# Performance work log

Hardware: AMD Instinct MI355X
Metric: run time of the kernel (lower is better)

Reference implementation:

```python
import jax, jax.numpy as jnp
import numpy as np

D = 512            # model size
H = 8              # num_heads
HD = D // H        # head_size = 64
WIN = 7            # num_keys (payload tokens per window)
QNB = 5            # query_nb for 'mean' aggregation
SCALE = D ** -0.5  # NOTE: torch module scales by size**-0.5, not head_size**-0.5
EPS = 1e-5


def setup_inputs() -> dict:
    key = jax.random.key(0)
    ks = jax.random.split(key, 12)
    B, M = 8, 4096
    w = lambda i: jax.random.normal(ks[i], (D, D), jnp.float32) * 0.02
    return {
        "k": jax.random.normal(ks[0], (B, M, D), jnp.float32),
        "v": jax.random.normal(ks[1], (B, M, D), jnp.float32),
        "q": jax.random.normal(ks[2], (B, M, D), jnp.float32),
        "query_len": 3584,
        "Wk": w(3), "bk": jnp.zeros((D,), jnp.float32),
        "Wv": w(4), "bv": jnp.zeros((D,), jnp.float32),
        "Wq": w(5), "bq": jnp.zeros((D,), jnp.float32),
        "ln_g": jnp.ones((D,), jnp.float32), "ln_b": jnp.zeros((D,), jnp.float32),
        "Wpq": w(6), "bpq": jnp.zeros((D,), jnp.float32),
        "Wpk": w(7), "bpk": jnp.zeros((D,), jnp.float32),
        "Wo": w(8), "bo": jnp.zeros((D,), jnp.float32),
    }


def reference(k, v, q, query_len, Wk, bk, Wv, bv, Wq, bq, ln_g, ln_b, Wpq, bpq, Wpk, bpk, Wo, bo):
    B, M, _ = k.shape
    win_num = -(-query_len // WIN)     # ceil
    per_win = M // win_num

    k = k @ Wk + bk
    v = v @ Wv + bv
    q = q @ Wq + bq

    # 'mean' query aggregation: AvgPool1d(kernel=QNB, stride=1, pad=QNB//2),
    # count_include_pad=True => always divide by QNB (zero-padded)
    qp = jnp.pad(q, ((0, 0), (QNB // 2, QNB // 2), (0, 0)))
    q = sum(qp[:, j:j + M] for j in range(QNB)) / QNB

    # ---- stage 1: DSA (local attention inside each window of per_win tokens)
    resh = lambda x: x.reshape(B, win_num, per_win, H, HD).transpose(0, 1, 3, 2, 4)
    dq, dk, dv = resh(q), resh(k), resh(v)                       # [B,W,H,p,hd]
    attn = jax.nn.softmax(jnp.einsum('bwhqd,bwhkd->bwhqk', dq, dk) * SCALE, axis=-1)
    out = jnp.einsum('bwhqk,bwhkd->bwhqd', attn, dv)
    out = out.transpose(0, 1, 3, 2, 4).reshape(B, win_num, per_win, D)

    win_tok = out[:, :, 0, :]          # [B, W, D] window summary tokens
    attn_x = out[:, :, 1:, :]

    # LayerNorm + exact GELU on window tokens
    mu = win_tok.mean(-1, keepdims=True)
    var = ((win_tok - mu) ** 2).mean(-1, keepdims=True)
    win_tok = (win_tok - mu) / jnp.sqrt(var + EPS) * ln_g + ln_b
    win_tok = jax.nn.gelu(win_tok, approximate=False)

    # ---- stage 2: PSA (attention over window summary tokens)
    pq = (win_tok @ Wpq + bpq).reshape(B, win_num, H, HD).transpose(0, 2, 1, 3)  # [B,H,W,hd]
    pk = (win_tok @ Wpk + bpk).reshape(B, win_num, H, HD).transpose(0, 2, 1, 3)
    pv = attn_x.reshape(B, win_num, WIN, H, HD).transpose(0, 3, 1, 2, 4)
    pv = pv.reshape(B, H, win_num, WIN * HD)

    pattn = jax.nn.softmax(jnp.einsum('bhqd,bhkd->bhqk', pq, pk) * SCALE, axis=-1)
    pout = jnp.einsum('bhqk,bhkd->bhqd', pattn, pv)
    pout = pout.transpose(0, 2, 1, 3).reshape(B, win_num, H, WIN, HD)
    pout = pout.transpose(0, 1, 3, 2, 4).reshape(B, win_num, WIN, D)

    out = (pout + attn_x).reshape(B, win_num * WIN, D)[:, :query_len, :]
    return out @ Wo + bo
```

## Files before the change

kernel.cpp:

```cpp
#include <hip/hip_runtime.h>
#include <hip/hip_bf16.h>
#include <math.h>

#define SCALE_ 0.04419417382415922f
#define EPS_  1e-5f

typedef unsigned short u16;
typedef __attribute__((ext_vector_type(8))) short     bf16x8;
typedef __attribute__((ext_vector_type(4))) float     f32x4;
typedef __attribute__((ext_vector_type(8))) unsigned short u16x8;
typedef __attribute__((ext_vector_type(4))) unsigned short u16x4;

__device__ __forceinline__ u16 f2b(float f) {
  union { float f; unsigned int u; } x; x.f = f;
  unsigned int u = x.u;
  return (u16)((u + 0x7FFFu + ((u >> 16) & 1u)) >> 16);
}
__device__ __forceinline__ float b2f(u16 h) {
  union { unsigned int u; float f; } x; x.u = ((unsigned int)h) << 16;
  return x.f;
}
__device__ __forceinline__ void gload_lds16(const void* g, void* l) {
  __builtin_amdgcn_global_load_lds(
      (const __attribute__((address_space(1))) void*)g,
      (__attribute__((address_space(3))) void*)l, 16, 0, 0);
}

__global__ __launch_bounds__(256) void wconv(
    const float* W0, const float* W1, const float* W2,
    const float* W3, const float* W4, const float* W5, u16* wt)
{
  const float* W;
  switch (blockIdx.z) {
    case 0: W = W0; break; case 1: W = W1; break; case 2: W = W2; break;
    case 3: W = W3; break; case 4: W = W4; break; default: W = W5; break;
  }
  u16* Wt = wt + (size_t)blockIdx.z * 262144;
  const int k0 = blockIdx.x * 64, n0 = blockIdx.y * 64;
  __shared__ float T[64][68];
  const int tid = threadIdx.x;
#pragma unroll
  for (int it = 0; it < 4; ++it) {
    int L = it * 256 + tid;
    int r = L >> 4, cg = L & 15;
    float4 v = *reinterpret_cast<const float4*>(W + (size_t)(k0 + r) * 512 + n0 + cg * 4);
    T[r][cg * 4 + 0] = v.x; T[r][cg * 4 + 1] = v.y;
    T[r][cg * 4 + 2] = v.z; T[r][cg * 4 + 3] = v.w;
  }
  __syncthreads();
#pragma unroll
  for (int it = 0; it < 2; ++it) {
    int L = it * 256 + tid;
    int rn = L >> 3, kg = L & 7;
    u16x8 o;
#pragma unroll
    for (int e = 0; e < 8; ++e) o[e] = f2b(T[kg * 8 + e][rn]);
    *(u16x8*)(Wt + (size_t)(n0 + rn) * 512 + k0 + kg * 8) = o;
  }
}

__global__ __launch_bounds__(512) void gemm_proj(
    const float* A0, const u16* Bt0, const float* bi0, u16* C0,
    const float* A1, const u16* Bt1, const float* bi1, u16* C1,
    const float* A2, const u16* Bt2, const float* bi2, u16* C2)
{
  const float *A, *bias; const u16* Bt; u16* C;
  if (blockIdx.z == 0)      { A = A0; Bt = Bt0; bias = bi0; C = C0; }
  else if (blockIdx.z == 1) { A = A1; Bt = Bt1; bias = bi1; C = C1; }
  else                      { A = A2; Bt = Bt2; bias = bi2; C = C2; }

  __shared__ u16 As[8192];
  __shared__ u16 Bs[32768];
  const int tid = threadIdx.x;
  const int lane = tid & 63, wid = tid >> 6;
  const int wr = wid >> 2, wcn = wid & 3;
  const int l15 = lane & 15, lh = lane >> 4, l7 = lane & 7;
  const int m0 = blockIdx.x * 128;

  const f32x4 fz = {0.f, 0.f, 0.f, 0.f};
  f32x4 acc[4][8];
#pragma unroll
  for (int m = 0; m < 4; ++m)
#pragma unroll
    for (int n = 0; n < 8; ++n) acc[m][n] = fz;

  int aoff[2], boff[2];
#pragma unroll
  for (int kh = 0; kh < 2; ++kh) {
    int slot = ((kh * 4 + lh) ^ l7) << 4;
    aoff[kh] = (wr * 64 + l15) * 128 + slot;
    boff[kh] = (wcn * 128 + l15) * 128 + slot;
  }

  for (int k0 = 0; k0 < 512; k0 += 64) {
    __syncthreads();
#pragma unroll
    for (int it = 0; it < 8; ++it) {
      int L = it * 512 + tid;
      int r = L >> 3, s = L & 7;
      int c = s ^ (r & 7);
      gload_lds16(Bt + (size_t)r * 512 + k0 + c * 8,
                  (char*)Bs + (it * 512 + wid * 64) * 16);
    }
    float4 xa[2], xb[2];
#pragma unroll
    for (int it = 0; it < 2; ++it) {
      int L = it * 512 + tid;
      int r = L >> 3, s = L & 7;
      int c = s ^ (r & 7);
      const float* ga = A + (size_t)(m0 + r) * 512 + k0 + c * 8;
      xa[it] = *reinterpret_cast<const float4*>(ga);
      xb[it] = *reinterpret_cast<const float4*>(ga + 4);
    }
#pragma unroll
    for (int it = 0; it < 2; ++it) {
      int L = it * 512 + tid;
      u16x8 o;
      o[0] = f2b(xa[it].x); o[1] = f2b(xa[it].y);
      o[2] = f2b(xa[it].z); o[3] = f2b(xa[it].w);
      o[4] = f2b(xb[it].x); o[5] = f2b(xb[it].y);
      o[6] = f2b(xb[it].z); o[7] = f2b(xb[it].w);
      *(u16x8*)((char*)As + L * 16) = o;
    }
    __syncthreads();
#pragma unroll
    for (int kh = 0; kh < 2; ++kh) {
      bf16x8 af[4], bfr[8];
#pragma unroll
      for (int m = 0; m < 4; ++m)
        af[m] = *(const bf16x8*)((const char*)As + aoff[kh] + m * 2048);
#pragma unroll
      for (int n = 0; n < 8; ++n)
        bfr[n] = *(const bf16x8*)((const char*)Bs + boff[kh] + n * 2048);
#pragma unroll
      for (int m = 0; m < 4; ++m)
#pragma unroll
        for (int n = 0; n < 8; ++n)
          acc[m][n] = __builtin_amdgcn_mfma_f32_16x16x32_bf16(af[m], bfr[n], acc[m][n], 0, 0, 0);
    }
  }

  const int gn0 = wcn * 128 + l15;
  float bv[8];
#pragma unroll
  for (int n = 0; n < 8; ++n) bv[n] = bias[gn0 + n * 16];
#pragma unroll
  for (int m = 0; m < 4; ++m)
#pragma unroll
    for (int reg = 0; reg < 4; ++reg) {
      int gm = m0 + wr * 64 + m * 16 + lh * 4 + reg;
#pragma unroll
      for (int n = 0; n < 8; ++n)
        C[(size_t)gm * 512 + gn0 + n * 16] = f2b(acc[m][n][reg] + bv[n]);
    }
}

__global__ __launch_bounds__(512) void gemm_out(
    const u16* __restrict__ A, const u16* __restrict__ Bt,
    const float* __restrict__ bias, float* __restrict__ C)
{
  __shared__ u16 As[2][4096];
  __shared__ u16 Bs[2][16384];
  const int tid = threadIdx.x;
  const int lane = tid & 63, wid = tid >> 6;
  const int wr = wid >> 2, wcn = wid & 3;
  const int l15 = lane & 15, lh = lane >> 4;
  const int sx = (l15 >> 1) & 3;
  const int m0 = blockIdx.x * 128;
  const int rr = tid >> 2, sp = tid & 3;
  const int ssw = sp ^ ((rr >> 1) & 3);

  const f32x4 fz = {0.f, 0.f, 0.f, 0.f};
  f32x4 acc[4][8];
#pragma unroll
  for (int m = 0; m < 4; ++m)
#pragma unroll
    for (int n = 0; n < 8; ++n) acc[m][n] = fz;

  const int aoff0 = (wr * 64 + l15) * 64 + ((lh ^ sx) << 4);
  const int boff0 = (wcn * 128 + l15) * 64 + ((lh ^ sx) << 4);

  {
#pragma unroll
    for (int it = 0; it < 4; ++it)
      gload_lds16(Bt + (size_t)(it * 128 + rr) * 512 + ssw * 8,
                  (char*)Bs[0] + (it * 512 + wid * 64) * 16);
    gload_lds16(A + (size_t)(m0 + rr) * 512 + ssw * 8,
                (char*)As[0] + (wid * 64) * 16);
  }
  __syncthreads();

#pragma unroll 2
  for (int t = 0; t < 16; ++t) {
    const int cur = t & 1, nxt = cur ^ 1;
    if (t < 15) {
      const int k0 = (t + 1) * 32;
#pragma unroll
      for (int it = 0; it < 4; ++it)
        gload_lds16(Bt + (size_t)(it * 128 + rr) * 512 + k0 + ssw * 8,
                    (char*)Bs[nxt] + (it * 512 + wid * 64) * 16);
      gload_lds16(A + (size_t)(m0 + rr) * 512 + k0 + ssw * 8,
                  (char*)As[nxt] + (wid * 64) * 16);
    }
    bf16x8 af[4], bfr[8];
#pragma unroll
    for (int m = 0; m < 4; ++m)
      af[m] = *(const bf16x8*)((const char*)As[cur] + aoff0 + m * 1024);
#pragma unroll
    for (int n = 0; n < 8; ++n)
      bfr[n] = *(const bf16x8*)((const char*)Bs[cur] + boff0 + n * 1024);
#pragma unroll
    for (int m = 0; m < 4; ++m)
#pragma unroll
      for (int n = 0; n < 8; ++n)
        acc[m][n] = __builtin_amdgcn_mfma_f32_16x16x32_bf16(af[m], bfr[n], acc[m][n], 0, 0, 0);
    __syncthreads();
  }

  const int gn0 = wcn * 128 + l15;
  float bv[8];
#pragma unroll
  for (int n = 0; n < 8; ++n) bv[n] = bias[gn0 + n * 16];
#pragma unroll
  for (int m = 0; m < 4; ++m)
#pragma unroll
    for (int reg = 0; reg < 4; ++reg) {
      int gm = m0 + wr * 64 + m * 16 + lh * 4 + reg;
#pragma unroll
      for (int n = 0; n < 8; ++n)
        C[(size_t)gm * 512 + gn0 + n * 16] = acc[m][n][reg] + bv[n];
    }
}

__global__ __launch_bounds__(256) void gemm_pp(
    const u16* __restrict__ A,
    const u16* __restrict__ Bt0, const float* __restrict__ bi0, u16* __restrict__ C0,
    const u16* __restrict__ Bt1, const float* __restrict__ bi1, u16* __restrict__ C1)
{
  const u16* Bt; const float* bias; u16* C;
  if (blockIdx.z == 0) { Bt = Bt0; bias = bi0; C = C0; }
  else                 { Bt = Bt1; bias = bi1; C = C1; }

  __shared__ u16 As[8192];
  __shared__ u16 Bs[8192];
  const int tid = threadIdx.x;
  const int lane = tid & 63, wid = tid >> 6;
  const int wr = wid >> 1, wc = wid & 1;
  const int l15 = lane & 15, lh = lane >> 4, l7 = lane & 7;
  const int m0 = blockIdx.x * 128, n0 = blockIdx.y * 128;

  const f32x4 fz = {0.f, 0.f, 0.f, 0.f};
  f32x4 acc[4][4];
#pragma unroll
  for (int m = 0; m < 4; ++m)
#pragma unroll
    for (int n = 0; n < 4; ++n) acc[m][n] = fz;

  int aoff[2], boff[2];
#pragma unroll
  for (int kh = 0; kh < 2; ++kh) {
    int slot = ((kh * 4 + lh) ^ l7) << 4;
    aoff[kh] = (wr * 64 + l15) * 128 + slot;
    boff[kh] = (wc * 64 + l15) * 128 + slot;
  }

  for (int k0 = 0; k0 < 512; k0 += 64) {
    __syncthreads();
#pragma unroll
    for (int it = 0; it < 4; ++it) {
      int L = it * 256 + tid;
      int r = L >> 3, s = L & 7;
      int c = s ^ (r & 7);
      gload_lds16(A  + (size_t)(m0 + r) * 512 + k0 + c * 8,
                  (char*)As + (it * 256 + wid * 64) * 16);
      gload_lds16(Bt + (size_t)(n0 + r) * 512 + k0 + c * 8,
                  (char*)Bs + (it * 256 + wid * 64) * 16);
    }
    __syncthreads();
#pragma unroll
    for (int kh = 0; kh < 2; ++kh) {
      bf16x8 af[4], bfr[4];
#pragma unroll
      for (int m = 0; m < 4; ++m)
        af[m] = *(const bf16x8*)((const char*)As + aoff[kh] + m * 2048);
#pragma unroll
      for (int n = 0; n < 4; ++n)
        bfr[n] = *(const bf16x8*)((const char*)Bs + boff[kh] + n * 2048);
#pragma unroll
      for (int m = 0; m < 4; ++m)
#pragma unroll
        for (int n = 0; n < 4; ++n)
          acc[m][n] = __builtin_amdgcn_mfma_f32_16x16x32_bf16(af[m], bfr[n], acc[m][n], 0, 0, 0);
    }
  }

  const int gn0 = n0 + wc * 64 + l15;
  float bv[4];
#pragma unroll
  for (int n = 0; n < 4; ++n) bv[n] = bias[gn0 + n * 16];
#pragma unroll
  for (int m = 0; m < 4; ++m)
#pragma unroll
    for (int reg = 0; reg < 4; ++reg) {
      int gm = m0 + wr * 64 + m * 16 + lh * 4 + reg;
#pragma unroll
      for (int n = 0; n < 4; ++n)
        C[(size_t)gm * 512 + gn0 + n * 16] = f2b(acc[m][n][reg] + bv[n]);
    }
}

__global__ __launch_bounds__(256) void qk_mfma(
    const u16* __restrict__ pq, const u16* __restrict__ pk,
    u16* __restrict__ expS, float* __restrict__ rsumP)
{
  __shared__ u16 As[8192];
  __shared__ u16 Bs[8192];
  const int tid = threadIdx.x;
  const int lane = tid & 63, wid = tid >> 6;
  const int wr = wid >> 1, wc = wid & 1;
  const int l15 = lane & 15, lh = lane >> 4, l7 = lane & 7;
  const int bh = blockIdx.x & 63;
  const int sidx = blockIdx.x >> 6;
  const int b = bh >> 3, h = bh & 7;
  const int wq0 = (sidx & 3) * 128, wk0 = (sidx >> 2) * 128;

  const f32x4 fz = {0.f, 0.f, 0.f, 0.f};
  f32x4 acc[4][4];
#pragma unroll
  for (int m = 0; m < 4; ++m)
#pragma unroll
    for (int n = 0; n < 4; ++n) acc[m][n] = fz;

#pragma unroll
  for (int it = 0; it < 4; ++it) {
    int L = it * 256 + tid;
    int r = L >> 3, s = L & 7;
    int c = s ^ (r & 7);
    gload_lds16(pq + ((size_t)b * 512 + wq0 + r) * 512 + h * 64 + c * 8,
                (char*)As + (it * 256 + wid * 64) * 16);
    gload_lds16(pk + ((size_t)b * 512 + wk0 + r) * 512 + h * 64 + c * 8,
                (char*)Bs + (it * 256 + wid * 64) * 16);
  }
  __syncthreads();

#pragma unroll
  for (int kh = 0; kh < 2; ++kh) {
    int slot = ((kh * 4 + lh) ^ l7) << 4;
    int aoff = (wr * 64 + l15) * 128 + slot;
    int boff = (wc * 64 + l15) * 128 + slot;
    bf16x8 af[4], bfr[4];
#pragma unroll
    for (int m = 0; m < 4; ++m)
      af[m] = *(const bf16x8*)((const char*)As + aoff + m * 2048);
#pragma unroll
    for (int n = 0; n < 4; ++n)
      bfr[n] = *(const bf16x8*)((const char*)Bs + boff + n * 2048);
#pragma unroll
    for (int m = 0; m < 4; ++m)
#pragma unroll
      for (int n = 0; n < 4; ++n)
        acc[m][n] = __builtin_amdgcn_mfma_f32_16x16x32_bf16(af[m], bfr[n], acc[m][n], 0, 0, 0);
  }

  const int gn0 = wk0 + wc * 64 + l15;
  float rs[4][4];
#pragma unroll
  for (int m = 0; m < 4; ++m)
#pragma unroll
    for (int reg = 0; reg < 4; ++reg) {
      int gm = wq0 + wr * 64 + m * 16 + lh * 4 + reg;
      float rsum = 0.0f;
#pragma unroll
      for (int n = 0; n < 4; ++n) {
        float e = expf(acc[m][n][reg] * SCALE_);
        rsum += e;
        expS[((size_t)bh * 512 + gm) * 512 + gn0 + n * 16] = f2b(e);
      }
      rs[m][reg] = rsum;
    }

#pragma unroll
  for (int m = 0; m < 4; ++m)
#pragma unroll
    for (int reg = 0; reg < 4; ++reg) {
      float v = rs[m][reg];
      v += __shfl_xor(v, 1);
      v += __shfl_xor(v, 2);
      v += __shfl_xor(v, 4);
      v += __shfl_xor(v, 8);
      rs[m][reg] = v;
    }
  if (l15 == 0) {
    const int p = (wk0 >> 6) + wc;
#pragma unroll
    for (int m = 0; m < 4; ++m)
#pragma unroll
      for (int reg = 0; reg < 4; ++reg) {
        int gm = wq0 + wr * 64 + m * 16 + lh * 4 + reg;
        rsumP[((size_t)bh * 8 + p) * 512 + gm] = rs[m][reg];
      }
  }
}

__global__ __launch_bounds__(64) void attn_win(
    const u16* kp, const u16* vp, const u16* qp0, u16* attn)
{
  const int h = blockIdx.x, w = blockIdx.y, b = blockIdx.z;
  const int t = threadIdx.x;
  __shared__ float ks[8][68], vs[8][68], qr[12][68], qs[8][68], Ps[8][9];
  const size_t base = ((size_t)b * 4096 + (size_t)w * 8) * 512 + h * 64;

  {
    int i = t >> 3, dg = t & 7;
    u16x8 kv = *(const u16x8*)(kp + base + (size_t)i * 512 + dg * 8);
    u16x8 vv = *(const u16x8*)(vp + base + (size_t)i * 512 + dg * 8);
#pragma unroll
    for (int e = 0; e < 8; ++e) {
      ks[i][dg * 8 + e] = b2f(kv[e]);
      vs[i][dg * 8 + e] = b2f(vv[e]);
    }
  }
#pragma unroll
  for (int l = 0; l < 2; ++l) {
    int L = t + l * 64;
    if (L < 96) {
      int i = L >> 3, dg = L & 7;
      int m = w * 8 - 2 + i;
      if (m >= 0 && m < 4096) {
        u16x8 qv = *(const u16x8*)(qp0 + ((size_t)b * 4096 + m) * 512 + h * 64 + dg * 8);
#pragma unroll
        for (int e = 0; e < 8; ++e) qr[i][dg * 8 + e] = b2f(qv[e]);
      } else {
#pragma unroll
        for (int e = 0; e < 8; ++e) qr[i][dg * 8 + e] = 0.0f;
      }
    }
  }
  __syncthreads();
#pragma unroll
  for (int j = 0; j < 8; ++j)
    qs[j][t] = 0.2f * (qr[j][t] + qr[j + 1][t] + qr[j + 2][t] + qr[j + 3][t] + qr[j + 4][t]);
  __syncthreads();

  const int qi = t >> 3, kj = t & 7;
  float s = 0.0f;
#pragma unroll
  for (int d = 0; d < 64; ++d) s = fmaf(qs[qi][d], ks[kj][d], s);
  s *= SCALE_;
  float mx = s;
  mx = fmaxf(mx, __shfl_xor(mx, 1));
  mx = fmaxf(mx, __shfl_xor(mx, 2));
  mx = fmaxf(mx, __shfl_xor(mx, 4));
  float e = expf(s - mx);
  float sum = e;
  sum += __shfl_xor(sum, 1);
  sum += __shfl_xor(sum, 2);
  sum += __shfl_xor(sum, 4);
  Ps[qi][kj] = e / sum;
  __syncthreads();

  float o[8];
#pragma unroll
  for (int c = 0; c < 8; ++c) o[c] = 0.0f;
#pragma unroll
  for (int tt = 0; tt < 8; ++tt) {
    float pw = Ps[qi][tt];
#pragma unroll
    for (int c = 0; c < 8; ++c) o[c] = fmaf(pw, vs[tt][kj * 8 + c], o[c]);
  }
  u16x8 ov;
#pragma unroll
  for (int c = 0; c < 8; ++c) ov[c] = f2b(o[c]);
  *(u16x8*)(attn + base + (size_t)qi * 512 + kj * 8) = ov;
}

__global__ __launch_bounds__(256) void pvt_build(const u16* attn, u16* pvT)
{
  const int bh = blockIdx.x;
  const int b = bh >> 3, h = bh & 7;
  const int w0 = blockIdx.y * 32;
  __shared__ u16 TL[448 * 40];
  const int tid = threadIdx.x;
#pragma unroll
  for (int it = 0; it < 8; ++it) {
    int L = it * 256 + tid;
    int dg = L & 7, r = L >> 3;
    int w2l = r >> 3, tt = r & 7;
    if (tt < 7) {
      int m = 8 * (w0 + w2l) + tt + 1;
      u16x8 v = *(const u16x8*)(attn + ((size_t)b * 4096 + m) * 512 + h * 64 + dg * 8);
#pragma unroll
      for (int e = 0; e < 8; ++e)
        TL[(tt * 64 + dg * 8 + e) * 40 + w2l] = v[e];
    }
  }
  __syncthreads();
#pragma unroll
  for (int it = 0; it < 7; ++it) {
    int L = it * 256 + tid;
    int n = L >> 2, seg = L & 3;
    u16x8 v = *(const u16x8*)(&TL[n * 40 + seg * 8]);
    *(u16x8*)(pvT + ((size_t)bh * 448 + n) * 512 + w0 + seg * 8) = v;
  }
}

__global__ __launch_bounds__(64) void ln_gelu(
    const u16* attn, const float* g, const float* be, u16* wt)
{
  const int r = blockIdx.x;
  const int b = r >> 9, w = r & 511;
  const int t = threadIdx.x;
  const u16* x = attn + (((size_t)b * 4096) + (size_t)w * 8) * 512;

  u16x8 v = *(const u16x8*)(x + t * 8);
  float xv[8];
  float s1 = 0.f, s2 = 0.f;
#pragma unroll
  for (int e = 0; e < 8; ++e) {
    xv[e] = b2f(v[e]);
    s1 += xv[e]; s2 += xv[e] * xv[e];
  }
#pragma unroll
  for (int off = 1; off < 64; off <<= 1) {
    s1 += __shfl_xor(s1, off);
    s2 += __shfl_xor(s2, off);
  }
  const float mu  = s1 * (1.0f / 512.0f);
  const float var = s2 * (1.0f / 512.0f) - mu * mu;
  const float inv = 1.0f / sqrtf(var + EPS_);

  const int d0 = t * 8;
  float4 g0 = *reinterpret_cast<const float4*>(g + d0);
  float4 g1 = *reinterpret_cast<const float4*>(g + d0 + 4);
  float4 b0 = *reinterpret_cast<const float4*>(be + d0);
  float4 b1 = *reinterpret_cast<const float4*>(be + d0 + 4);
  float gv[8] = {g0.x, g0.y, g0.z, g0.w, g1.x, g1.y, g1.z, g1.w};
  float bvv[8] = {b0.x, b0.y, b0.z, b0.w, b1.x, b1.y, b1.z, b1.w};
  const float k2 = 0.70710678118654752f;
  u16x8 ov;
#pragma unroll
  for (int e = 0; e < 8; ++e) {
    float y = (xv[e] - mu) * inv * gv[e] + bvv[e];
    ov[e] = f2b(0.5f * y * (1.0f + erff(y * k2)));
  }
  *(u16x8*)(wt + (size_t)r * 512 + d0) = ov;
}

__global__ __launch_bounds__(256) void rs_inv(const float* rsumP, float* rsinv)
{
  const int row = blockIdx.x * 256 + threadIdx.x;
  const int bh = row >> 9, wq = row & 511;
  float s = 0.f;
#pragma unroll
  for (int p = 0; p < 8; ++p)
    s += rsumP[((size_t)bh * 8 + p) * 512 + wq];
  rsinv[row] = 1.0f / s;
}

__global__ __launch_bounds__(256) void pv_mfma(
    const u16* __restrict__ expS, const u16* __restrict__ pvT,
    const float* __restrict__ rsinv, const u16* __restrict__ attn,
    u16* __restrict__ X2)
{
  __shared__ u16 As[8192];
  __shared__ u16 Bs[4096];
  const int tid = threadIdx.x;
  const int lane = tid & 63, wid = tid >> 6;
  const int wr = wid >> 1, wc = wid & 1;
  const int l15 = lane & 15, lh = lane >> 4, l7 = lane & 7;
  const int nt  = blockIdx.x >> 8;
  const int idx = blockIdx.x & 255;
  const int m0 = (idx & 3) * 128;
  const int bh = idx >> 2, b = bh >> 3, h = bh & 7;

  const f32x4 fz = {0.f, 0.f, 0.f, 0.f};
  f32x4 acc[4][2];
#pragma unroll
  for (int m = 0; m < 4; ++m)
#pragma unroll
    for (int n = 0; n < 2; ++n) acc[m][n] = fz;

  int aoff[2], boff[2];
#pragma unroll
  for (int kh = 0; kh < 2; ++kh) {
    int slot = ((kh * 4 + lh) ^ l7) << 4;
    aoff[kh] = (wr * 64 + l15) * 128 + slot;
    boff[kh] = (wc * 32 + l15) * 128 + slot;
  }

  for (int k0 = 0; k0 < 512; k0 += 64) {
    __syncthreads();
#pragma unroll
    for (int it = 0; it < 4; ++it) {
      int L = it * 256 + tid;
      int r = L >> 3, s = L & 7;
      int c = s ^ (r & 7);
      gload_lds16(expS + ((size_t)bh * 512 + m0 + r) * 512 + k0 + c * 8,
                  (char*)As + (it * 256 + wid * 64) * 16);
    }
#pragma unroll
    for (int it = 0; it < 2; ++it) {
      int L = it * 256 + tid;
      int r = L >> 3, s = L & 7;
      int c = s ^ (r & 7);
      gload_lds16(pvT + ((size_t)bh * 448 + nt * 64 + r) * 512 + k0 + c * 8,
                  (char*)Bs + (it * 256 + wid * 64) * 16);
    }
    __syncthreads();
#pragma unroll
    for (int kh = 0; kh < 2; ++kh) {
      bf16x8 af[4], bfr[2];
#pragma unroll
      for (int m = 0; m < 4; ++m)
        af[m] = *(const bf16x8*)((const char*)As + aoff[kh] + m * 2048);
#pragma unroll
      for (int n = 0; n < 2; ++n)
        bfr[n] = *(const bf16x8*)((const char*)Bs + boff[kh] + n * 2048);
#pragma unroll
      for (int m = 0; m < 4; ++m)
#pragma unroll
        for (int n = 0; n < 2; ++n)
          acc[m][n] = __builtin_amdgcn_mfma_f32_16x16x32_bf16(af[m], bfr[n], acc[m][n], 0, 0, 0);
    }
  }

#pragma unroll
  for (int m = 0; m < 4; ++m)
#pragma unroll
    for (int reg = 0; reg < 4; ++reg) {
      int gm = m0 + wr * 64 + m * 16 + lh * 4 + reg;
      float ri = rsinv[bh * 512 + gm];
#pragma unroll
      for (int n = 0; n < 2; ++n) {
        int d = wc * 32 + n * 16 + l15;
        float res = b2f(attn[((size_t)b * 4096 + gm * 8 + nt + 1) * 512 + h * 64 + d]);
        X2[((size_t)b * 3584 + gm * 7 + nt) * 512 + h * 64 + d] =
            f2b(acc[m][n][reg] * ri + res);
      }
    }
}

extern "C" void kernel_launch(void* const* d_in, const int* in_sizes, int n_in,
                              void* d_out, int out_size, void* d_ws, size_t ws_size,
                              hipStream_t stream)
{
  const float* k_in = (const float*)d_in[0];
  const float* v_in = (const float*)d_in[1];
  const float* q_in = (const float*)d_in[2];
  const float* Wk  = (const float*)d_in[4];
  const float* bk  = (const float*)d_in[5];
  const float* Wv  = (const float*)d_in[6];
  const float* bv  = (const float*)d_in[7];
  const float* Wq  = (const float*)d_in[8];
  const float* bq  = (const float*)d_in[9];
  const float* lng = (const float*)d_in[10];
  const float* lnb = (const float*)d_in[11];
  const float* Wpq = (const float*)d_in[12];
  const float* bpq = (const float*)d_in[13];
  const float* Wpk = (const float*)d_in[14];
  const float* bpk = (const float*)d_in[15];
  const float* Wo  = (const float*)d_in[16];
  const float* bo  = (const float*)d_in[17];
  float* out = (float*)d_out;

  char* ws = (char*)d_ws;
  const size_t MB = 1024 * 1024;
  u16* wtb  = (u16*)(ws);
  u16* kp   = (u16*)(ws + 16 * MB);
  u16* vp   = (u16*)(ws + 52 * MB);
  u16* qp0  = (u16*)(ws + 88 * MB);
  u16* attn = (u16*)(ws + 124 * MB);
  u16*   wt    = (u16*)(ws + 16 * MB);
  u16*   pq    = (u16*)(ws + 20 * MB);
  u16*   pk    = (u16*)(ws + 28 * MB);
  float* rsinv = (float*)(ws + 36 * MB);
  float* rsumP = (float*)(ws + 37 * MB);
  u16*   expS  = (u16*)(ws + 40 * MB);
  u16*   pvT   = (u16*)(ws + 76 * MB);
  u16*   X2    = (u16*)(ws + 160 * MB);

  u16* Wkt  = wtb;
  u16* Wvt  = wtb + 1 * 262144;
  u16* Wqt  = wtb + 2 * 262144;
  u16* Wpqt = wtb + 3 * 262144;
  u16* Wpkt = wtb + 4 * 262144;
  u16* Wot  = wtb + 5 * 262144;

  wconv<<<dim3(8, 8, 6), 256, 0, stream>>>(Wk, Wv, Wq, Wpq, Wpk, Wo, wtb);

  gemm_proj<<<dim3(256, 1, 3), 512, 0, stream>>>(
      k_in, Wkt, bk, kp,
      v_in, Wvt, bv, vp,
      q_in, Wqt, bq, qp0);

  attn_win<<<dim3(8, 512, 8), 64, 0, stream>>>(kp, vp, qp0, attn);
  pvt_build<<<dim3(64, 16), 256, 0, stream>>>(attn, pvT);
  ln_gelu<<<4096, 64, 0, stream>>>(attn, lng, lnb, wt);

  gemm_pp<<<dim3(32, 4, 2), 256, 0, stream>>>(
      wt, Wpqt, bpq, pq, Wpkt, bpk, pk);

  qk_mfma<<<1024, 256, 0, stream>>>(pq, pk, expS, rsumP);
  rs_inv<<<128, 256, 0, stream>>>(rsumP, rsinv);
  pv_mfma<<<1792, 256, 0, stream>>>(expS, pvT, rsinv, attn, X2);

  gemm_out<<<dim3(224, 1, 1), 512, 0, stream>>>(X2, Wot, bo, out);
}
```

Measured before the change: 278.0 us.

## Fuse PSA QK, softmax normalization and PV into one flash-style kernel

Replaces the three-kernel PSA stage (QK^T with exp written to global, row-sum reduction, P·V matmul) with a single fused kernel. Each block holds 128 query rows, loops over key tiles of 64, computes exp scores into LDS, then multiplies by the corresponding pvT tile, and normalizes by the row sum at the end. This avoids writing and re-reading the 32 MB bf16 expS buffer and removes two launches. In exchange, the grid shrinks to 256 blocks of 512 threads using about 96 KB of LDS each, with three barriers per key tile. No max subtraction is used, the same as before.

```diff
diff --git a/kernel.cpp b/kernel.cpp
--- a/kernel.cpp
+++ b/kernel.cpp
@@ -309,97 +309,134 @@
     }
 }
 
-__global__ __launch_bounds__(256) void qk_mfma(
+__global__ __launch_bounds__(512) void pattn(
     const u16* __restrict__ pq, const u16* __restrict__ pk,
-    u16* __restrict__ expS, float* __restrict__ rsumP)
-{
-  __shared__ u16 As[8192];
-  __shared__ u16 Bs[8192];
+    const u16* __restrict__ pvT, const u16* __restrict__ attn,
+    u16* __restrict__ X2)
+{
+  __shared__ u16 Aq[8192];
+  __shared__ u16 Bk[4096];
+  __shared__ u16 Pl[8192];
+  __shared__ u16 Vt[28672];
+  __shared__ float rsl[128];
+
   const int tid = threadIdx.x;
   const int lane = tid & 63, wid = tid >> 6;
-  const int wr = wid >> 1, wc = wid & 1;
+  const int wr = wid >> 2, wcn = wid & 3;
   const int l15 = lane & 15, lh = lane >> 4, l7 = lane & 7;
   const int bh = blockIdx.x & 63;
-  const int sidx = blockIdx.x >> 6;
+  const int wq0 = (blockIdx.x >> 6) * 128;
   const int b = bh >> 3, h = bh & 7;
-  const int wq0 = (sidx & 3) * 128, wk0 = (sidx >> 2) * 128;
 
   const f32x4 fz = {0.f, 0.f, 0.f, 0.f};
-  f32x4 acc[4][4];
-#pragma unroll
-  for (int m = 0; m < 4; ++m)
-#pragma unroll
-    for (int n = 0; n < 4; ++n) acc[m][n] = fz;
-
-#pragma unroll
-  for (int it = 0; it < 4; ++it) {
-    int L = it * 256 + tid;
+  f32x4 acc[4][7];
+#pragma unroll
+  for (int m = 0; m < 4; ++m)
+#pragma unroll
+    for (int n = 0; n < 7; ++n) acc[m][n] = fz;
+  float rs4[4] = {0.f, 0.f, 0.f, 0.f};
+
+#pragma unroll
+  for (int it = 0; it < 2; ++it) {
+    int L = it * 512 + tid;
     int r = L >> 3, s = L & 7;
     int c = s ^ (r & 7);
     gload_lds16(pq + ((size_t)b * 512 + wq0 + r) * 512 + h * 64 + c * 8,
-                (char*)As + (it * 256 + wid * 64) * 16);
-    gload_lds16(pk + ((size_t)b * 512 + wk0 + r) * 512 + h * 64 + c * 8,
-                (char*)Bs + (it * 256 + wid * 64) * 16);
+                (char*)Aq + L * 16);
+  }
+
+  int slotk[2];
+#pragma unroll
+  for (int kh = 0; kh < 2; ++kh) slotk[kh] = ((kh * 4 + lh) ^ l7) << 4;
+
+  for (int wk0 = 0; wk0 < 512; wk0 += 64) {
+    {
+      int L = tid;
+      int r = L >> 3, s = L & 7;
+      int c = s ^ (r & 7);
+      gload_lds16(pk + ((size_t)b * 512 + wk0 + r) * 512 + h * 64 + c * 8,
+                  (char*)Bk + L * 16);
+    }
+#pragma unroll
+    for (int it = 0; it < 7; ++it) {
+      int L = it * 512 + tid;
+      int r = L >> 3, s = L & 7;
+      int c = s ^ (r & 7);
+      gload_lds16(pvT + ((size_t)bh * 448 + r) * 512 + wk0 + c * 8,
+                  (char*)Vt + L * 16);
+    }
+    __syncthreads();
+
+    f32x4 pacc[4];
+#pragma unroll
+    for (int n = 0; n < 4; ++n) pacc[n] = fz;
+#pragma unroll
+    for (int kh = 0; kh < 2; ++kh) {
+      bf16x8 af = *(const bf16x8*)((const char*)Aq + (wid * 16 + l15) * 128 + slotk[kh]);
+#pragma unroll
+      for (int n = 0; n < 4; ++n) {
+        bf16x8 bfr = *(const bf16x8*)((const char*)Bk + (n * 16 + l15) * 128 + slotk[kh]);
+        pacc[n] = __builtin_amdgcn_mfma_f32_16x16x32_bf16(af, bfr, pacc[n], 0, 0, 0);
+      }
+    }
+#pragma unroll
+    for (int n = 0; n < 4; ++n)
+#pragma unroll
+      for (int reg = 0; reg < 4; ++reg) {
+        float e = expf(pacc[n][reg] * SCALE_);
+        rs4[reg] += e;
+        int prow = wid * 16 + lh * 4 + reg;
+        int pcol = n * 16 + l15;
+        int phys = (pcol >> 3) ^ (prow & 7);
+        *(u16*)((char*)Pl + prow * 128 + phys * 16 + (pcol & 7) * 2) = f2b(e);
+      }
+    __syncthreads();
+
+#pragma unroll
+    for (int kh = 0; kh < 2; ++kh) {
+      bf16x8 af[4], bfr[7];
+#pragma unroll
+      for (int m = 0; m < 4; ++m)
+        af[m] = *(const bf16x8*)((const char*)Pl + (wr * 64 + m * 16 + l15) * 128 + slotk[kh]);
+#pragma unroll
+      for (int n = 0; n < 7; ++n)
+        bfr[n] = *(const bf16x8*)((const char*)Vt + (wcn * 112 + n * 16 + l15) * 128 + slotk[kh]);
+#pragma unroll
+      for (int m = 0; m < 4; ++m)
+#pragma unroll
+        for (int n = 0; n < 7; ++n)
+          acc[m][n] = __builtin_amdgcn_mfma_f32_16x16x32_bf16(af[m], bfr[n], acc[m][n], 0, 0, 0);
+    }
+    __syncthreads();
+  }
+
+#pragma unroll
+  for (int reg = 0; reg < 4; ++reg) {
+    float v = rs4[reg];
+    v += __shfl_xor(v, 1);
+    v += __shfl_xor(v, 2);
+    v += __shfl_xor(v, 4);
+    v += __shfl_xor(v, 8);
+    if (l15 == 0) rsl[wid * 16 + lh * 4 + reg] = v;
   }
   __syncthreads();
 
 #pragma unroll
-  for (int kh = 0; kh < 2; ++kh) {
-    int slot = ((kh * 4 + lh) ^ l7) << 4;
-    int aoff = (wr * 64 + l15) * 128 + slot;
-    int boff = (wc * 64 + l15) * 128 + slot;
-    bf16x8 af[4], bfr[4];
-#pragma unroll
-    for (int m = 0; m < 4; ++m)
-      af[m] = *(const bf16x8*)((const char*)As + aoff + m * 2048);
-#pragma unroll
-    for (int n = 0; n < 4; ++n)
-      bfr[n] = *(const bf16x8*)((const char*)Bs + boff + n * 2048);
-#pragma unroll
-    for (int m = 0; m < 4; ++m)
-#pragma unroll
-      for (int n = 0; n < 4; ++n)
-        acc[m][n] = __builtin_amdgcn_mfma_f32_16x16x32_bf16(af[m], bfr[n], acc[m][n], 0, 0, 0);
-  }
-
-  const int gn0 = wk0 + wc * 64 + l15;
-  float rs[4][4];
-#pragma unroll
   for (int m = 0; m < 4; ++m)
 #pragma unroll
     for (int reg = 0; reg < 4; ++reg) {
-      int gm = wq0 + wr * 64 + m * 16 + lh * 4 + reg;
-      float rsum = 0.0f;
-#pragma unroll
-      for (int n = 0; n < 4; ++n) {
-        float e = expf(acc[m][n][reg] * SCALE_);
-        rsum += e;
-        expS[((size_t)bh * 512 + gm) * 512 + gn0 + n * 16] = f2b(e);
+      int lrow = wr * 64 + m * 16 + lh * 4 + reg;
+      int gm = wq0 + lrow;
+      float ri = 1.0f / rsl[lrow];
+#pragma unroll
+      for (int n = 0; n < 7; ++n) {
+        int nd = wcn * 112 + n * 16 + l15;
+        int nt = nd >> 6, d = nd & 63;
+        float res = b2f(attn[((size_t)b * 4096 + gm * 8 + nt + 1) * 512 + h * 64 + d]);
+        X2[((size_t)b * 3584 + gm * 7 + nt) * 512 + h * 64 + d] =
+            f2b(acc[m][n][reg] * ri + res);
       }
-      rs[m][reg] = rsum;
-    }
-
-#pragma unroll
-  for (int m = 0; m < 4; ++m)
-#pragma unroll
-    for (int reg = 0; reg < 4; ++reg) {
-      float v = rs[m][reg];
-      v += __shfl_xor(v, 1);
-      v += __shfl_xor(v, 2);
-      v += __shfl_xor(v, 4);
-      v += __shfl_xor(v, 8);
-      rs[m][reg] = v;
-    }
-  if (l15 == 0) {
-    const int p = (wk0 >> 6) + wc;
-#pragma unroll
-    for (int m = 0; m < 4; ++m)
-#pragma unroll
-      for (int reg = 0; reg < 4; ++reg) {
-        int gm = wq0 + wr * 64 + m * 16 + lh * 4 + reg;
-        rsumP[((size_t)bh * 8 + p) * 512 + gm] = rs[m][reg];
-      }
-  }
+    }
 }
 
 __global__ __launch_bounds__(64) void attn_win(
@@ -544,100 +581,6 @@
     ov[e] = f2b(0.5f * y * (1.0f + erff(y * k2)));
   }
   *(u16x8*)(wt + (size_t)r * 512 + d0) = ov;
-}
-
-__global__ __launch_bounds__(256) void rs_inv(const float* rsumP, float* rsinv)
-{
-  const int row = blockIdx.x * 256 + threadIdx.x;
-  const int bh = row >> 9, wq = row & 511;
-  float s = 0.f;
-#pragma unroll
-  for (int p = 0; p < 8; ++p)
-    s += rsumP[((size_t)bh * 8 + p) * 512 + wq];
-  rsinv[row] = 1.0f / s;
-}
-
-__global__ __launch_bounds__(256) void pv_mfma(
-    const u16* __restrict__ expS, const u16* __restrict__ pvT,
-    const float* __restrict__ rsinv, const u16* __restrict__ attn,
-    u16* __restrict__ X2)
-{
-  __shared__ u16 As[8192];
-  __shared__ u16 Bs[4096];
-  const int tid = threadIdx.x;
-  const int lane = tid & 63, wid = tid >> 6;
-  const int wr = wid >> 1, wc = wid & 1;
-  const int l15 = lane & 15, lh = lane >> 4, l7 = lane & 7;
-  const int nt  = blockIdx.x >> 8;
-  const int idx = blockIdx.x & 255;
-  const int m0 = (idx & 3) * 128;
-  const int bh = idx >> 2, b = bh >> 3, h = bh & 7;
-
-  const f32x4 fz = {0.f, 0.f, 0.f, 0.f};
-  f32x4 acc[4][2];
-#pragma unroll
-  for (int m = 0; m < 4; ++m)
-#pragma unroll
-    for (int n = 0; n < 2; ++n) acc[m][n] = fz;
-
-  int aoff[2], boff[2];
-#pragma unroll
-  for (int kh = 0; kh < 2; ++kh) {
-    int slot = ((kh * 4 + lh) ^ l7) << 4;
-    aoff[kh] = (wr * 64 + l15) * 128 + slot;
-    boff[kh] = (wc * 32 + l15) * 128 + slot;
-  }
-
-  for (int k0 = 0; k0 < 512; k0 += 64) {
-    __syncthreads();
-#pragma unroll
-    for (int it = 0; it < 4; ++it) {
-      int L = it * 256 + tid;
-      int r = L >> 3, s = L & 7;
-      int c = s ^ (r & 7);
-      gload_lds16(expS + ((size_t)bh * 512 + m0 + r) * 512 + k0 + c * 8,
-                  (char*)As + (it * 256 + wid * 64) * 16);
-    }
-#pragma unroll
-    for (int it = 0; it < 2; ++it) {
-      int L = it * 256 + tid;
-      int r = L >> 3, s = L & 7;
-      int c = s ^ (r & 7);
-      gload_lds16(pvT + ((size_t)bh * 448 + nt * 64 + r) * 512 + k0 + c * 8,
-                  (char*)Bs + (it * 256 + wid * 64) * 16);
-    }
-    __syncthreads();
-#pragma unroll
-    for (int kh = 0; kh < 2; ++kh) {
-      bf16x8 af[4], bfr[2];
-#pragma unroll
-      for (int m = 0; m < 4; ++m)
-        af[m] = *(const bf16x8*)((const char*)As + aoff[kh] + m * 2048);
-#pragma unroll
-      for (int n = 0; n < 2; ++n)
-        bfr[n] = *(const bf16x8*)((const char*)Bs + boff[kh] + n * 2048);
-#pragma unroll
-      for (int m = 0; m < 4; ++m)
-#pragma unroll
-        for (int n = 0; n < 2; ++n)
-          acc[m][n] = __builtin_amdgcn_mfma_f32_16x16x32_bf16(af[m], bfr[n], acc[m][n], 0, 0, 0);
-    }
-  }
-
-#pragma unroll
-  for (int m = 0; m < 4; ++m)
-#pragma unroll
-    for (int reg = 0; reg < 4; ++reg) {
-      int gm = m0 + wr * 64 + m * 16 + lh * 4 + reg;
-      float ri = rsinv[bh * 512 + gm];
-#pragma unroll
-      for (int n = 0; n < 2; ++n) {
-        int d = wc * 32 + n * 16 + l15;
-        float res = b2f(attn[((size_t)b * 4096 + gm * 8 + nt + 1) * 512 + h * 64 + d]);
-        X2[((size_t)b * 3584 + gm * 7 + nt) * 512 + h * 64 + d] =
-            f2b(acc[m][n][reg] * ri + res);
-      }
-    }
 }
 
 extern "C" void kernel_launch(void* const* d_in, const int* in_sizes, int n_in,
@@ -673,9 +616,6 @@
   u16*   wt    = (u16*)(ws + 16 * MB);
   u16*   pq    = (u16*)(ws + 20 * MB);
   u16*   pk    = (u16*)(ws + 28 * MB);
-  float* rsinv = (float*)(ws + 36 * MB);
-  float* rsumP = (float*)(ws + 37 * MB);
-  u16*   expS  = (u16*)(ws + 40 * MB);
   u16*   pvT   = (u16*)(ws + 76 * MB);
   u16*   X2    = (u16*)(ws + 160 * MB);
 
@@ -700,9 +640,7 @@
   gemm_pp<<<dim3(32, 4, 2), 256, 0, stream>>>(
       wt, Wpqt, bpq, pq, Wpkt, bpk, pk);
 
-  qk_mfma<<<1024, 256, 0, stream>>>(pq, pk, expS, rsumP);
-  rs_inv<<<128, 256, 0, stream>>>(rsumP, rsinv);
-  pv_mfma<<<1792, 256, 0, stream>>>(expS, pvT, rsinv, attn, X2);
+  pattn<<<256, 512, 0, stream>>>(pq, pk, pvT, attn, X2);
 
   gemm_out<<<dim3(224, 1, 1), 512, 0, stream>>>(X2, Wot, bo, out);
 }
```

After: 256.5 us (median of 3 runs). 1.08x faster.
